# Optimization experiments

Measured on AMD Instinct MI355X. Metric: run time of the kernel, lower is better.

The kernel has to match this reference:

```python
import jax, jax.numpy as jnp
import numpy as np
from jax.ops import segment_sum

N_NODES = 50000
N_EDGES = 800000
IN_CH = 128
HID = 256
N_CLASSES = 10
N_GRAPHS = 64


def setup_inputs() -> dict:
    key = jax.random.key(0)
    ks = jax.random.split(key, 12)
    x = jax.random.normal(ks[0], (N_NODES, IN_CH), dtype=jnp.float32)
    edge_index = jax.random.randint(ks[1], (2, N_EDGES), 0, N_NODES, dtype=jnp.int64)
    batch = jnp.sort(jax.random.randint(ks[2], (N_NODES,), 0, N_GRAPHS, dtype=jnp.int64))
    def glorot(k, shape):
        lim = (6.0 / (shape[0] + shape[1])) ** 0.5
        return jax.random.uniform(k, shape, jnp.float32, -lim, lim)
    # GraphConv has two linear maps: lin_rel (neighbor aggregate, with bias) and lin_root (self)
    params = {
        "W1_root": glorot(ks[3], (IN_CH, HID)),  "W1_nbr": glorot(ks[4], (IN_CH, HID)),  "b1": jnp.zeros((HID,), jnp.float32),
        "W2_root": glorot(ks[5], (HID, HID)),    "W2_nbr": glorot(ks[6], (HID, HID)),    "b2": jnp.zeros((HID,), jnp.float32),
        "W3_root": glorot(ks[7], (HID, HID)),    "W3_nbr": glorot(ks[8], (HID, HID)),    "b3": jnp.zeros((HID,), jnp.float32),
        "W_lin": glorot(ks[9], (HID, N_CLASSES)), "b_lin": jnp.zeros((N_CLASSES,), jnp.float32),
    }
    return {"x": x, "edge_index": edge_index, "batch": batch, **params}


def _graph_conv(x, src, dst, W_root, W_nbr, b):
    # out_i = W_root x_i + W_nbr * sum_{j: (j->i) in E} x_j + b   (PyG GraphConv, aggr='add')
    agg = segment_sum(x[src], dst, num_segments=N_NODES)  # [N, d]
    return x @ W_root + agg @ W_nbr + b


def reference(x, edge_index, batch,
              W1_root, W1_nbr, b1,
              W2_root, W2_nbr, b2,
              W3_root, W3_nbr, b3,
              W_lin, b_lin):
    src, dst = edge_index[0], edge_index[1]
    h = jax.nn.relu(_graph_conv(x, src, dst, W1_root, W1_nbr, b1))
    h = jax.nn.relu(_graph_conv(h, src, dst, W2_root, W2_nbr, b2))
    h = _graph_conv(h, src, dst, W3_root, W3_nbr, b3)
    # global_mean_pool over graph ids
    sums = segment_sum(h, batch, num_segments=N_GRAPHS)                        # [G, HID]
    counts = segment_sum(jnp.ones((h.shape[0],), h.dtype), batch, num_segments=N_GRAPHS)
    pooled = sums / jnp.maximum(counts, 1.0)[:, None]
    # dropout is identity at inference
    return pooled @ W_lin + b_lin  # [G, n_classes]
```

## Files before the change

### kernel.cpp

```cpp
#include <hip/hip_runtime.h>
#include <stdint.h>

#define N_NODES 50000
#define N_EDGES 800000
#define IN_CH 128
#define HID 256
#define N_GRAPHS 64
#define N_CLASSES 10

#define GEMM_WG ((N_NODES + 127) / 128)
#define NB ((N_NODES + 127) / 128)
#define EPB 4096
#define CAP 4096

typedef unsigned short u16;
typedef __attribute__((ext_vector_type(8))) short short8;
typedef __attribute__((ext_vector_type(4))) float f32x4;

__device__ __forceinline__ float bf2f(uint32_t u) {
    union { uint32_t i; float f; } v; v.i = u << 16; return v.f;
}
__device__ __forceinline__ uint32_t f2bf(float f) {
    union { float f; uint32_t i; } v; v.f = f;
    return (v.i + 0x7FFFu + ((v.i >> 16) & 1u)) >> 16;
}

__global__ void __launch_bounds__(512) bin_pass(const int* __restrict__ src,
                                                const int* __restrict__ dst,
                                                int* __restrict__ gcnt,
                                                uint32_t* __restrict__ tmp)
{
    __shared__ int hist[NB];
    __shared__ int base[NB];
    int t = threadIdx.x;
    for (int i = t; i < NB; i += 512) hist[i] = 0;
    __syncthreads();
    const int e0 = blockIdx.x * EPB;
    int b_[8], s_[8], d_[8];
    #pragma unroll
    for (int k = 0; k < 8; ++k) {
        int e = e0 + k * 512 + t;
        if (e < N_EDGES) {
            int d = dst[e];
            b_[k] = d >> 7;
            d_[k] = d & 127;
            s_[k] = src[e];
            atomicAdd(&hist[b_[k]], 1);
        } else b_[k] = -1;
    }
    __syncthreads();
    for (int i = t; i < NB; i += 512) {
        int c = hist[i];
        base[i] = c ? atomicAdd(&gcnt[i], c) : 0;
        hist[i] = 0;
    }
    __syncthreads();
    #pragma unroll
    for (int k = 0; k < 8; ++k) {
        if (b_[k] >= 0) {
            int r = atomicAdd(&hist[b_[k]], 1);
            int pos = base[b_[k]] + r;
            if (pos < CAP)
                tmp[(size_t)b_[k] * CAP + pos] = ((uint32_t)s_[k] << 7) | (uint32_t)d_[k];
        }
    }
}

__global__ void __launch_bounds__(512) bucket_scan(const int* __restrict__ gcnt,
                                                   int* __restrict__ boff,
                                                   int* __restrict__ row_start)
{
    __shared__ int buf[512];
    int t = threadIdx.x;
    int v = (t < NB) ? gcnt[t] : 0;
    buf[t] = v;
    __syncthreads();
    #pragma unroll
    for (int off = 1; off < 512; off <<= 1) {
        int a = (t >= off) ? buf[t - off] : 0;
        __syncthreads();
        buf[t] += a;
        __syncthreads();
    }
    if (t < NB) boff[t] = buf[t] - v;
    if (t == 0) row_start[N_NODES] = N_EDGES;
}

__global__ void __launch_bounds__(256) debin2(const uint32_t* __restrict__ tmp,
                                              const int* __restrict__ gcnt,
                                              const int* __restrict__ boff,
                                              int* __restrict__ row_start,
                                              int* __restrict__ esrc)
{
    __shared__ int h[128];
    __shared__ int pre[128];
    __shared__ int cur[128];
    const int b = blockIdx.x;
    const int n0 = b * 128;
    const int nn = min(128, N_NODES - n0);
    const int t = threadIdx.x;
    const int cnt = min(gcnt[b], CAP);
    const int bb = boff[b];
    const uint32_t* te = tmp + (size_t)b * CAP;

    if (t < 128) h[t] = 0;
    __syncthreads();
    for (int p = t; p < cnt; p += 256)
        atomicAdd(&h[te[p] & 127u], 1);
    __syncthreads();
    if (t < 128) pre[t] = h[t];
    __syncthreads();
    #pragma unroll
    for (int off = 1; off < 128; off <<= 1) {
        int a = (t >= off && t < 128) ? pre[t - off] : 0;
        __syncthreads();
        if (t < 128) pre[t] += a;
        __syncthreads();
    }
    if (t < nn) {
        int rs = bb + pre[t] - h[t];
        row_start[n0 + t] = rs;
        cur[t] = rs;
    }
    __syncthreads();
    for (int p = t; p < cnt; p += 256) {
        uint32_t v = te[p];
        int pos = atomicAdd(&cur[v & 127u], 1);
        esrc[pos] = (int)(v >> 7);
    }
}

#define XB 3125
__global__ void __launch_bounds__(256)
cvt_all(const float* __restrict__ x, u16* __restrict__ xb,
        const float* __restrict__ W1r, const float* __restrict__ W1n,
        const float* __restrict__ W2r, const float* __restrict__ W2n,
        const float* __restrict__ W3r, const float* __restrict__ W3n,
        u16* __restrict__ o1r, u16* __restrict__ o1n,
        u16* __restrict__ o2r, u16* __restrict__ o2n,
        u16* __restrict__ o3r, u16* __restrict__ o3n)
{
    if (blockIdx.x < XB) {
        int id = blockIdx.x * 256 + threadIdx.x;
        const float4 a = *reinterpret_cast<const float4*>(x + (size_t)id * 8);
        const float4 b = *reinterpret_cast<const float4*>(x + (size_t)id * 8 + 4);
        uint4 o;
        o.x = f2bf(a.x) | (f2bf(a.y) << 16);
        o.y = f2bf(a.z) | (f2bf(a.w) << 16);
        o.z = f2bf(b.x) | (f2bf(b.y) << 16);
        o.w = f2bf(b.z) | (f2bf(b.w) << 16);
        *reinterpret_cast<uint4*>(xb + (size_t)id * 8) = o;
        return;
    }
    int id = (blockIdx.x - XB) * 256 + threadIdx.x;
    if (id < 65536) {
        int m = id >> 15;
        int r = id & 32767;
        int k = r >> 8, n = r & 255;
        const float* W = m ? W1n : W1r;
        u16* O = m ? o1n : o1r;
        O[n * 128 + k] = (u16)f2bf(W[r]);
    } else {
        id -= 65536;
        int m = id >> 16;
        int r = id & 65535;
        int k = r >> 8, n = r & 255;
        const float* W = (m == 0) ? W2r : (m == 1) ? W2n : (m == 2) ? W3r : W3n;
        u16* O = (m == 0) ? o2r : (m == 1) ? o2n : (m == 2) ? o3r : o3n;
        O[n * 256 + k] = (u16)f2bf(W[r]);
    }
}

template<int D, int NPH>
__global__ void __launch_bounds__(256)
gather_ph(const u16* __restrict__ feat, const int* __restrict__ row_start,
          const int* __restrict__ esrc, u16* __restrict__ agg)
{
    constexpr int CW = D / NPH;
    constexpr int GS = CW / 8;
    constexpr int NPB = 256 / GS;
    const int node = blockIdx.x * NPB + threadIdx.x / GS;
    const int lane = threadIdx.x % GS;
    const bool act = node < N_NODES;
    int s = 0, e = 0;
    if (act) { s = row_start[node]; e = row_start[node + 1]; }

    #pragma unroll
    for (int p = 0; p < NPH; ++p) {
        const u16* fp = feat + p * CW + lane * 8;
        float acc[8] = {0.f, 0.f, 0.f, 0.f, 0.f, 0.f, 0.f, 0.f};
        auto add = [&](uint4 v) {
            acc[0] += bf2f(v.x & 0xFFFF); acc[1] += bf2f(v.x >> 16);
            acc[2] += bf2f(v.y & 0xFFFF); acc[3] += bf2f(v.y >> 16);
            acc[4] += bf2f(v.z & 0xFFFF); acc[5] += bf2f(v.z >> 16);
            acc[6] += bf2f(v.w & 0xFFFF); acc[7] += bf2f(v.w >> 16);
        };
        int j = s;
        for (; j + 3 < e; j += 4) {
            int s0 = esrc[j], s1 = esrc[j + 1], s2 = esrc[j + 2], s3 = esrc[j + 3];
            uint4 v0 = *reinterpret_cast<const uint4*>(fp + (size_t)s0 * D);
            uint4 v1 = *reinterpret_cast<const uint4*>(fp + (size_t)s1 * D);
            uint4 v2 = *reinterpret_cast<const uint4*>(fp + (size_t)s2 * D);
            uint4 v3 = *reinterpret_cast<const uint4*>(fp + (size_t)s3 * D);
            add(v0); add(v1); add(v2); add(v3);
        }
        for (; j < e; ++j) {
            uint4 v0 = *reinterpret_cast<const uint4*>(fp + (size_t)esrc[j] * D);
            add(v0);
        }
        if (act) {
            uint4 o;
            o.x = f2bf(acc[0]) | (f2bf(acc[1]) << 16);
            o.y = f2bf(acc[2]) | (f2bf(acc[3]) << 16);
            o.z = f2bf(acc[4]) | (f2bf(acc[5]) << 16);
            o.w = f2bf(acc[6]) | (f2bf(acc[7]) << 16);
            *reinterpret_cast<uint4*>(agg + (size_t)node * D + p * CW + lane * 8) = o;
        }
        if (p + 1 < NPH) __syncthreads();
    }
}

template<int RELU>
__global__ void __launch_bounds__(512)
mfma_gemm(const u16* __restrict__ A1, const u16* __restrict__ A2,
          const u16* __restrict__ B1t, const u16* __restrict__ B2t,
          const float* __restrict__ bias,
          u16* __restrict__ C,
          int M, int K)
{
    __shared__ __align__(16) u16 As[128][40];
    __shared__ __align__(16) u16 Bs[256][40];

    const int orig = blockIdx.x;
    const int q = GEMM_WG / 8, r = GEMM_WG % 8;
    const int xcd = orig % 8;
    const int wg = (xcd < r ? xcd * (q + 1) : r * (q + 1) + (xcd - r) * q) + orig / 8;

    const int tid = threadIdx.x;
    const int bm = wg * 128;
    const int w  = tid >> 6;
    const int wm = (w >> 2) * 64;
    const int wn = (w & 3) * 64;
    const int l  = tid & 63;
    const int lr = l & 15;
    const int kb = (l >> 4) * 8;

    f32x4 acc[4][4];
    #pragma unroll
    for (int i = 0; i < 4; ++i)
        #pragma unroll
        for (int j = 0; j < 4; ++j)
            acc[i][j] = (f32x4){0.f, 0.f, 0.f, 0.f};

    const int row_s = tid >> 2;
    const int c8    = (tid & 3) * 8;

    for (int mat = 0; mat < 2; ++mat) {
        const u16* __restrict__ Ag = mat ? A2 : A1;
        const u16* __restrict__ Bg = mat ? B2t : B1t;
        for (int k0 = 0; k0 < K; k0 += 32) {
            {
                uint4 va = make_uint4(0u, 0u, 0u, 0u);
                int gr = bm + row_s;
                if (gr < M)
                    va = *reinterpret_cast<const uint4*>(Ag + (size_t)gr * K + k0 + c8);
                *reinterpret_cast<uint4*>(&As[row_s][c8]) = va;
            }
            #pragma unroll
            for (int it = 0; it < 2; ++it) {
                int row = row_s + it * 128;
                uint4 vb = *reinterpret_cast<const uint4*>(Bg + (size_t)row * K + k0 + c8);
                *reinterpret_cast<uint4*>(&Bs[row][c8]) = vb;
            }
            __syncthreads();
            short8 af[4], bfr[4];
            #pragma unroll
            for (int f = 0; f < 4; ++f) {
                af[f]  = *reinterpret_cast<const short8*>(&As[wm + f * 16 + lr][kb]);
                bfr[f] = *reinterpret_cast<const short8*>(&Bs[wn + f * 16 + lr][kb]);
            }
            #pragma unroll
            for (int fm = 0; fm < 4; ++fm)
                #pragma unroll
                for (int fn = 0; fn < 4; ++fn)
                    acc[fm][fn] = __builtin_amdgcn_mfma_f32_16x16x32_bf16(
                        af[fm], bfr[fn], acc[fm][fn], 0, 0, 0);
            __syncthreads();
        }
    }

    const int r4 = (l >> 4) * 4;
    #pragma unroll
    for (int fm = 0; fm < 4; ++fm) {
        #pragma unroll
        for (int rr = 0; rr < 4; ++rr) {
            int row = bm + wm + fm * 16 + r4 + rr;
            if (row >= M) continue;
            #pragma unroll
            for (int fn = 0; fn < 4; ++fn) {
                int col = wn + fn * 16 + lr;
                float v = acc[fm][fn][rr] + bias[col];
                if (RELU) v = fmaxf(v, 0.f);
                C[(size_t)row * HID + col] = (u16)f2bf(v);
            }
        }
    }
}

__device__ __forceinline__ int lower_bound_g(const int* __restrict__ batch, int g)
{
    int lo = 0, hi = N_NODES;
    while (lo < hi) {
        int mid = (lo + hi) >> 1;
        if (batch[mid] < g) lo = mid + 1; else hi = mid;
    }
    return lo;
}

__global__ void pool1_kernel(const u16* __restrict__ h, const int* __restrict__ batch,
                             float* __restrict__ partial)
{
    int g = blockIdx.x >> 3;
    int c = blockIdx.x & 7;
    int t = threadIdx.x;
    int s = lower_bound_g(batch, g);
    int e = lower_bound_g(batch, g + 1);
    int cnt = e - s;
    int a = s + (int)(((long long)cnt * c) >> 3);
    int b = s + (int)(((long long)cnt * (c + 1)) >> 3);
    float acc = 0.f;
    for (int i = a; i < b; ++i)
        acc += bf2f(h[(size_t)i * HID + t]);
    partial[(size_t)blockIdx.x * HID + t] = acc;
}

__global__ void pool2_final(const float* __restrict__ partial, const int* __restrict__ batch,
                            const float* __restrict__ W_lin, const float* __restrict__ b_lin,
                            float* __restrict__ out)
{
    __shared__ float v[HID];
    int g = blockIdx.x;
    int t = threadIdx.x;
    float acc = 0.f;
    #pragma unroll
    for (int c = 0; c < 8; ++c)
        acc += partial[(size_t)(g * 8 + c) * HID + t];
    float cnt = fmaxf((float)(lower_bound_g(batch, g + 1) - lower_bound_g(batch, g)), 1.f);
    v[t] = acc / cnt;
    __syncthreads();
    if (t < N_CLASSES) {
        float s = b_lin[t];
        for (int k = 0; k < HID; ++k)
            s += v[k] * W_lin[k * N_CLASSES + t];
        out[g * N_CLASSES + t] = s;
    }
}

extern "C" void kernel_launch(void* const* d_in, const int* in_sizes, int n_in,
                              void* d_out, int out_size, void* d_ws, size_t ws_size,
                              hipStream_t stream)
{
    const float* x     = (const float*)d_in[0];
    const int*   ei    = (const int*)d_in[1];
    const int*   batch = (const int*)d_in[2];
    const float* W1r = (const float*)d_in[3];
    const float* W1n = (const float*)d_in[4];
    const float* b1  = (const float*)d_in[5];
    const float* W2r = (const float*)d_in[6];
    const float* W2n = (const float*)d_in[7];
    const float* b2  = (const float*)d_in[8];
    const float* W3r = (const float*)d_in[9];
    const float* W3n = (const float*)d_in[10];
    const float* b3  = (const float*)d_in[11];
    const float* Wl  = (const float*)d_in[12];
    const float* bl  = (const float*)d_in[13];
    float* out = (float*)d_out;

    const int* src = ei;
    const int* dst = ei + N_EDGES;

    char* base = (char*)d_ws;
    size_t off = 0;
    auto alloc = [&](size_t bytes) { char* p = base + off; off += (bytes + 255) & ~(size_t)255; return p; };
    u16* x_bf = (u16*)alloc((size_t)N_NODES * IN_CH * 2);
    u16* hA   = (u16*)alloc((size_t)N_NODES * HID * 2);
    u16* hB   = (u16*)alloc((size_t)N_NODES * HID * 2);
    u16* agg  = (u16*)alloc((size_t)N_NODES * HID * 2);
    u16* wt1r = (u16*)alloc((size_t)HID * IN_CH * 2);
    u16* wt1n = (u16*)alloc((size_t)HID * IN_CH * 2);
    u16* wt2r = (u16*)alloc((size_t)HID * HID * 2);
    u16* wt2n = (u16*)alloc((size_t)HID * HID * 2);
    u16* wt3r = (u16*)alloc((size_t)HID * HID * 2);
    u16* wt3n = (u16*)alloc((size_t)HID * HID * 2);
    float* partial = (float*)alloc((size_t)N_GRAPHS * 8 * HID * 4);
    int* row_start = (int*)alloc((size_t)(N_NODES + 1) * 4);
    int* esrc      = (int*)alloc((size_t)N_EDGES * 4);
    uint32_t* tmp  = (uint32_t*)alloc((size_t)NB * CAP * 4);
    int* gcnt      = (int*)alloc((size_t)NB * 4);
    int* boff      = (int*)alloc((size_t)NB * 4);

    hipMemsetAsync(gcnt, 0, NB * sizeof(int), stream);
    bin_pass<<<(N_EDGES + EPB - 1) / EPB, 512, 0, stream>>>(src, dst, gcnt, tmp);
    bucket_scan<<<1, 512, 0, stream>>>(gcnt, boff, row_start);
    debin2<<<NB, 256, 0, stream>>>(tmp, gcnt, boff, row_start, esrc);

    cvt_all<<<XB + 1280, 256, 0, stream>>>(x, x_bf, W1r, W1n, W2r, W2n, W3r, W3n,
                                           wt1r, wt1n, wt2r, wt2n, wt3r, wt3n);

    const int G128 = (N_NODES + 31) / 32;
    const int G256 = (N_NODES + 15) / 16;

    gather_ph<IN_CH, 2><<<G128, 256, 0, stream>>>(x_bf, row_start, esrc, agg);
    mfma_gemm<1><<<GEMM_WG, 512, 0, stream>>>(x_bf, agg, wt1r, wt1n, b1, hA, N_NODES, IN_CH);

    gather_ph<HID, 2><<<G256, 256, 0, stream>>>(hA, row_start, esrc, agg);
    mfma_gemm<1><<<GEMM_WG, 512, 0, stream>>>(hA, agg, wt2r, wt2n, b2, hB, N_NODES, HID);

    gather_ph<HID, 2><<<G256, 256, 0, stream>>>(hB, row_start, esrc, agg);
    mfma_gemm<0><<<GEMM_WG, 512, 0, stream>>>(hB, agg, wt3r, wt3n, b3, hA, N_NODES, HID);

    pool1_kernel<<<N_GRAPHS * 8, HID, 0, stream>>>(hA, batch, partial);
    pool2_final<<<N_GRAPHS, HID, 0, stream>>>(partial, batch, Wl, bl, out);
}
```

Before: 302.7 us.

## Store node features in blocked pair-chunk layout and split gather by column chunk

Node feature matrices are now stored in a blocked layout where two consecutive nodes share a 128-byte block per 32-column chunk. The gather kernel assigns each block a single 32-column chunk across 64 nodes, so each gathered neighbour read is a 64-byte contiguous piece, and concurrent blocks touch a smaller working set per chunk. The GEMMs read the root operand in blocked layout and, for the first two layers, write their output in blocked form. The costs are scattered 2-byte stores in the GEMM epilogue and more gather blocks that each reread the row_start and esrc lists.

New measurement: 344.0 us. +13.6%, slower.

```diff
diff --git a/kernel.cpp b/kernel.cpp
--- a/kernel.cpp
+++ b/kernel.cpp
@@ -12,6 +12,7 @@
 #define NB ((N_NODES + 127) / 128)
 #define EPB 4096
 #define CAP 4096
+#define GTILES ((N_NODES + 63) / 64)
 
 typedef unsigned short u16;
 typedef __attribute__((ext_vector_type(8))) short short8;
@@ -23,6 +24,10 @@
 __device__ __forceinline__ uint32_t f2bf(float f) {
     union { float f; uint32_t i; } v; v.f = f;
     return (v.i + 0x7FFFu + ((v.i >> 16) & 1u)) >> 16;
+}
+
+__device__ __forceinline__ size_t blk_idx(int node, int col, int nch) {
+    return ((size_t)(node >> 1) * nch + (col >> 5)) * 64 + (node & 1) * 32 + (col & 31);
 }
 
 __global__ void __launch_bounds__(512) bin_pass(const int* __restrict__ src,
@@ -132,7 +137,7 @@
 
 #define XB 3125
 __global__ void __launch_bounds__(256)
-cvt_all(const float* __restrict__ x, u16* __restrict__ xb,
+cvt_all(const float* __restrict__ x, u16* __restrict__ xblk,
         const float* __restrict__ W1r, const float* __restrict__ W1n,
         const float* __restrict__ W2r, const float* __restrict__ W2n,
         const float* __restrict__ W3r, const float* __restrict__ W3n,
@@ -142,6 +147,8 @@
 {
     if (blockIdx.x < XB) {
         int id = blockIdx.x * 256 + threadIdx.x;
+        int node = id >> 4;
+        int col0 = (id & 15) * 8;
         const float4 a = *reinterpret_cast<const float4*>(x + (size_t)id * 8);
         const float4 b = *reinterpret_cast<const float4*>(x + (size_t)id * 8 + 4);
         uint4 o;
@@ -149,7 +156,7 @@
         o.y = f2bf(a.z) | (f2bf(a.w) << 16);
         o.z = f2bf(b.x) | (f2bf(b.y) << 16);
         o.w = f2bf(b.z) | (f2bf(b.w) << 16);
-        *reinterpret_cast<uint4*>(xb + (size_t)id * 8) = o;
+        *reinterpret_cast<uint4*>(xblk + blk_idx(node, col0, IN_CH / 32)) = o;
         return;
     }
     int id = (blockIdx.x - XB) * 256 + threadIdx.x;
@@ -171,62 +178,57 @@
     }
 }
 
-template<int D, int NPH>
+template<int D>
 __global__ void __launch_bounds__(256)
-gather_ph(const u16* __restrict__ feat, const int* __restrict__ row_start,
-          const int* __restrict__ esrc, u16* __restrict__ agg)
-{
-    constexpr int CW = D / NPH;
-    constexpr int GS = CW / 8;
-    constexpr int NPB = 256 / GS;
-    const int node = blockIdx.x * NPB + threadIdx.x / GS;
-    const int lane = threadIdx.x % GS;
-    const bool act = node < N_NODES;
-    int s = 0, e = 0;
-    if (act) { s = row_start[node]; e = row_start[node + 1]; }
-
-    #pragma unroll
-    for (int p = 0; p < NPH; ++p) {
-        const u16* fp = feat + p * CW + lane * 8;
-        float acc[8] = {0.f, 0.f, 0.f, 0.f, 0.f, 0.f, 0.f, 0.f};
-        auto add = [&](uint4 v) {
-            acc[0] += bf2f(v.x & 0xFFFF); acc[1] += bf2f(v.x >> 16);
-            acc[2] += bf2f(v.y & 0xFFFF); acc[3] += bf2f(v.y >> 16);
-            acc[4] += bf2f(v.z & 0xFFFF); acc[5] += bf2f(v.z >> 16);
-            acc[6] += bf2f(v.w & 0xFFFF); acc[7] += bf2f(v.w >> 16);
-        };
-        int j = s;
-        for (; j + 3 < e; j += 4) {
-            int s0 = esrc[j], s1 = esrc[j + 1], s2 = esrc[j + 2], s3 = esrc[j + 3];
-            uint4 v0 = *reinterpret_cast<const uint4*>(fp + (size_t)s0 * D);
-            uint4 v1 = *reinterpret_cast<const uint4*>(fp + (size_t)s1 * D);
-            uint4 v2 = *reinterpret_cast<const uint4*>(fp + (size_t)s2 * D);
-            uint4 v3 = *reinterpret_cast<const uint4*>(fp + (size_t)s3 * D);
-            add(v0); add(v1); add(v2); add(v3);
-        }
-        for (; j < e; ++j) {
-            uint4 v0 = *reinterpret_cast<const uint4*>(fp + (size_t)esrc[j] * D);
-            add(v0);
-        }
-        if (act) {
-            uint4 o;
-            o.x = f2bf(acc[0]) | (f2bf(acc[1]) << 16);
-            o.y = f2bf(acc[2]) | (f2bf(acc[3]) << 16);
-            o.z = f2bf(acc[4]) | (f2bf(acc[5]) << 16);
-            o.w = f2bf(acc[6]) | (f2bf(acc[7]) << 16);
-            *reinterpret_cast<uint4*>(agg + (size_t)node * D + p * CW + lane * 8) = o;
-        }
-        if (p + 1 < NPH) __syncthreads();
-    }
-}
-
-template<int RELU>
+gather_blk(const u16* __restrict__ feat, const int* __restrict__ row_start,
+           const int* __restrict__ esrc, u16* __restrict__ agg)
+{
+    constexpr int NCH = D / 32;
+    const int chunk = blockIdx.x & (NCH - 1);
+    const int tile  = blockIdx.x / NCH;
+    const int node  = tile * 64 + (threadIdx.x >> 2);
+    const int lane  = threadIdx.x & 3;
+    if (node >= N_NODES) return;
+    const int s = row_start[node], e = row_start[node + 1];
+    float acc[8] = {0.f, 0.f, 0.f, 0.f, 0.f, 0.f, 0.f, 0.f};
+    const u16* fp = feat + (size_t)chunk * 64 + lane * 8;
+
+    auto addr = [&](int sj) {
+        return reinterpret_cast<const uint4*>(fp + ((size_t)(sj >> 1) * NCH) * 64 + (sj & 1) * 32);
+    };
+    auto add = [&](uint4 v) {
+        acc[0] += bf2f(v.x & 0xFFFF); acc[1] += bf2f(v.x >> 16);
+        acc[2] += bf2f(v.y & 0xFFFF); acc[3] += bf2f(v.y >> 16);
+        acc[4] += bf2f(v.z & 0xFFFF); acc[5] += bf2f(v.z >> 16);
+        acc[6] += bf2f(v.w & 0xFFFF); acc[7] += bf2f(v.w >> 16);
+    };
+
+    int j = s;
+    for (; j + 3 < e; j += 4) {
+        uint4 v0 = *addr(esrc[j]);
+        uint4 v1 = *addr(esrc[j + 1]);
+        uint4 v2 = *addr(esrc[j + 2]);
+        uint4 v3 = *addr(esrc[j + 3]);
+        add(v0); add(v1); add(v2); add(v3);
+    }
+    for (; j < e; ++j)
+        add(*addr(esrc[j]));
+
+    uint4 o;
+    o.x = f2bf(acc[0]) | (f2bf(acc[1]) << 16);
+    o.y = f2bf(acc[2]) | (f2bf(acc[3]) << 16);
+    o.z = f2bf(acc[4]) | (f2bf(acc[5]) << 16);
+    o.w = f2bf(acc[6]) | (f2bf(acc[7]) << 16);
+    *reinterpret_cast<uint4*>(agg + (size_t)node * D + chunk * 32 + lane * 8) = o;
+}
+
+template<int RELU, int K, int BLKOUT>
 __global__ void __launch_bounds__(512)
 mfma_gemm(const u16* __restrict__ A1, const u16* __restrict__ A2,
           const u16* __restrict__ B1t, const u16* __restrict__ B2t,
           const float* __restrict__ bias,
           u16* __restrict__ C,
-          int M, int K)
+          int M)
 {
     __shared__ __align__(16) u16 As[128][40];
     __shared__ __align__(16) u16 Bs[256][40];
@@ -262,8 +264,13 @@
             {
                 uint4 va = make_uint4(0u, 0u, 0u, 0u);
                 int gr = bm + row_s;
-                if (gr < M)
-                    va = *reinterpret_cast<const uint4*>(Ag + (size_t)gr * K + k0 + c8);
+                int col = k0 + c8;
+                if (gr < M) {
+                    if (mat == 0)
+                        va = *reinterpret_cast<const uint4*>(Ag + blk_idx(gr, col, K / 32));
+                    else
+                        va = *reinterpret_cast<const uint4*>(Ag + (size_t)gr * K + col);
+                }
                 *reinterpret_cast<uint4*>(&As[row_s][c8]) = va;
             }
             #pragma unroll
@@ -301,7 +308,10 @@
                 int col = wn + fn * 16 + lr;
                 float v = acc[fm][fn][rr] + bias[col];
                 if (RELU) v = fmaxf(v, 0.f);
-                C[(size_t)row * HID + col] = (u16)f2bf(v);
+                if (BLKOUT)
+                    C[blk_idx(row, col, HID / 32)] = (u16)f2bf(v);
+                else
+                    C[(size_t)row * HID + col] = (u16)f2bf(v);
             }
         }
     }
@@ -382,10 +392,10 @@
     char* base = (char*)d_ws;
     size_t off = 0;
     auto alloc = [&](size_t bytes) { char* p = base + off; off += (bytes + 255) & ~(size_t)255; return p; };
-    u16* x_bf = (u16*)alloc((size_t)N_NODES * IN_CH * 2);
-    u16* hA   = (u16*)alloc((size_t)N_NODES * HID * 2);
-    u16* hB   = (u16*)alloc((size_t)N_NODES * HID * 2);
-    u16* agg  = (u16*)alloc((size_t)N_NODES * HID * 2);
+    u16* x_blk = (u16*)alloc((size_t)N_NODES * IN_CH * 2);
+    u16* h1b   = (u16*)alloc((size_t)N_NODES * HID * 2);
+    u16* h2b   = (u16*)alloc((size_t)N_NODES * HID * 2);
+    u16* agg   = (u16*)alloc((size_t)N_NODES * HID * 2);
     u16* wt1r = (u16*)alloc((size_t)HID * IN_CH * 2);
     u16* wt1n = (u16*)alloc((size_t)HID * IN_CH * 2);
     u16* wt2r = (u16*)alloc((size_t)HID * HID * 2);
@@ -399,26 +409,25 @@
     int* gcnt      = (int*)alloc((size_t)NB * 4);
     int* boff      = (int*)alloc((size_t)NB * 4);
 
+    u16* h3 = h1b;
+
     hipMemsetAsync(gcnt, 0, NB * sizeof(int), stream);
     bin_pass<<<(N_EDGES + EPB - 1) / EPB, 512, 0, stream>>>(src, dst, gcnt, tmp);
     bucket_scan<<<1, 512, 0, stream>>>(gcnt, boff, row_start);
     debin2<<<NB, 256, 0, stream>>>(tmp, gcnt, boff, row_start, esrc);
 
-    cvt_all<<<XB + 1280, 256, 0, stream>>>(x, x_bf, W1r, W1n, W2r, W2n, W3r, W3n,
+    cvt_all<<<XB + 1280, 256, 0, stream>>>(x, x_blk, W1r, W1n, W2r, W2n, W3r, W3n,
                                            wt1r, wt1n, wt2r, wt2n, wt3r, wt3n);
 
-    const int G128 = (N_NODES + 31) / 32;
-    const int G256 = (N_NODES + 15) / 16;
-
-    gather_ph<IN_CH, 2><<<G128, 256, 0, stream>>>(x_bf, row_start, esrc, agg);
-    mfma_gemm<1><<<GEMM_WG, 512, 0, stream>>>(x_bf, agg, wt1r, wt1n, b1, hA, N_NODES, IN_CH);
-
-    gather_ph<HID, 2><<<G256, 256, 0, stream>>>(hA, row_start, esrc, agg);
-    mfma_gemm<1><<<GEMM_WG, 512, 0, stream>>>(hA, agg, wt2r, wt2n, b2, hB, N_NODES, HID);
-
-    gather_ph<HID, 2><<<G256, 256, 0, stream>>>(hB, row_start, esrc, agg);
-    mfma_gemm<0><<<GEMM_WG, 512, 0, stream>>>(hB, agg, wt3r, wt3n, b3, hA, N_NODES, HID);
-
-    pool1_kernel<<<N_GRAPHS * 8, HID, 0, stream>>>(hA, batch, partial);
+    gather_blk<IN_CH><<<GTILES * (IN_CH / 32), 256, 0, stream>>>(x_blk, row_start, esrc, agg);
+    mfma_gemm<1, IN_CH, 1><<<GEMM_WG, 512, 0, stream>>>(x_blk, agg, wt1r, wt1n, b1, h1b, N_NODES);
+
+    gather_blk<HID><<<GTILES * (HID / 32), 256, 0, stream>>>(h1b, row_start, esrc, agg);
+    mfma_gemm<1, HID, 1><<<GEMM_WG, 512, 0, stream>>>(h1b, agg, wt2r, wt2n, b2, h2b, N_NODES);
+
+    gather_blk<HID><<<GTILES * (HID / 32), 256, 0, stream>>>(h2b, row_start, esrc, agg);
+    mfma_gemm<0, HID, 0><<<GEMM_WG, 512, 0, stream>>>(h2b, agg, wt3r, wt3n, b3, h3, N_NODES);
+
+    pool1_kernel<<<N_GRAPHS * 8, HID, 0, stream>>>(h3, batch, partial);
     pool2_final<<<N_GRAPHS, HID, 0, stream>>>(partial, batch, Wl, bl, out);
 }
```

## Fuse neighbor gather into GEMM, keeping aggregates in shared memory

Applied to the files above, without the earlier changes.

Replaces the separate gather and dual-GEMM kernels per layer with one kernel. Each 64-row workgroup first gathers neighbor sums into shared memory, then runs the root and neighbor GEMMs, reading the aggregate straight from LDS. This drops the global write and re-read of the aggregate buffer and halves the launches per layer. In exchange the tile shrinks from 128 to 64 rows, so weight tiles are reloaded more often, and LDS use rises, which may limit occupancy. The gather phase also cannot overlap with MFMA work inside a block.

Result: slower. 329.3 us, median of 2 (+8.8%).

```diff
diff --git a/kernel.cpp b/kernel.cpp
--- a/kernel.cpp
+++ b/kernel.cpp
@@ -8,7 +8,7 @@
 #define N_GRAPHS 64
 #define N_CLASSES 10
 
-#define GEMM_WG ((N_NODES + 127) / 128)
+#define FUSED_WG ((N_NODES + 63) / 64)
 #define NB ((N_NODES + 127) / 128)
 #define EPB 4096
 #define CAP 4096
@@ -171,127 +171,150 @@
     }
 }
 
-template<int D, int NPH>
-__global__ void __launch_bounds__(256)
-gather_ph(const u16* __restrict__ feat, const int* __restrict__ row_start,
-          const int* __restrict__ esrc, u16* __restrict__ agg)
-{
-    constexpr int CW = D / NPH;
-    constexpr int GS = CW / 8;
-    constexpr int NPB = 256 / GS;
-    const int node = blockIdx.x * NPB + threadIdx.x / GS;
-    const int lane = threadIdx.x % GS;
-    const bool act = node < N_NODES;
-    int s = 0, e = 0;
-    if (act) { s = row_start[node]; e = row_start[node + 1]; }
-
-    #pragma unroll
-    for (int p = 0; p < NPH; ++p) {
-        const u16* fp = feat + p * CW + lane * 8;
-        float acc[8] = {0.f, 0.f, 0.f, 0.f, 0.f, 0.f, 0.f, 0.f};
-        auto add = [&](uint4 v) {
-            acc[0] += bf2f(v.x & 0xFFFF); acc[1] += bf2f(v.x >> 16);
-            acc[2] += bf2f(v.y & 0xFFFF); acc[3] += bf2f(v.y >> 16);
-            acc[4] += bf2f(v.z & 0xFFFF); acc[5] += bf2f(v.z >> 16);
-            acc[6] += bf2f(v.w & 0xFFFF); acc[7] += bf2f(v.w >> 16);
-        };
-        int j = s;
-        for (; j + 3 < e; j += 4) {
-            int s0 = esrc[j], s1 = esrc[j + 1], s2 = esrc[j + 2], s3 = esrc[j + 3];
-            uint4 v0 = *reinterpret_cast<const uint4*>(fp + (size_t)s0 * D);
-            uint4 v1 = *reinterpret_cast<const uint4*>(fp + (size_t)s1 * D);
-            uint4 v2 = *reinterpret_cast<const uint4*>(fp + (size_t)s2 * D);
-            uint4 v3 = *reinterpret_cast<const uint4*>(fp + (size_t)s3 * D);
-            add(v0); add(v1); add(v2); add(v3);
-        }
-        for (; j < e; ++j) {
-            uint4 v0 = *reinterpret_cast<const uint4*>(fp + (size_t)esrc[j] * D);
-            add(v0);
-        }
-        if (act) {
-            uint4 o;
-            o.x = f2bf(acc[0]) | (f2bf(acc[1]) << 16);
-            o.y = f2bf(acc[2]) | (f2bf(acc[3]) << 16);
-            o.z = f2bf(acc[4]) | (f2bf(acc[5]) << 16);
-            o.w = f2bf(acc[6]) | (f2bf(acc[7]) << 16);
-            *reinterpret_cast<uint4*>(agg + (size_t)node * D + p * CW + lane * 8) = o;
-        }
-        if (p + 1 < NPH) __syncthreads();
-    }
-}
-
-template<int RELU>
-__global__ void __launch_bounds__(512)
-mfma_gemm(const u16* __restrict__ A1, const u16* __restrict__ A2,
-          const u16* __restrict__ B1t, const u16* __restrict__ B2t,
-          const float* __restrict__ bias,
-          u16* __restrict__ C,
-          int M, int K)
-{
-    __shared__ __align__(16) u16 As[128][40];
+template<int RELU, int K>
+__global__ void __launch_bounds__(512, 4)
+fused_layer(const u16* __restrict__ feat,
+            const int* __restrict__ row_start,
+            const int* __restrict__ esrc,
+            const u16* __restrict__ B1t,
+            const u16* __restrict__ B2t,
+            const float* __restrict__ bias,
+            u16* __restrict__ C,
+            int M)
+{
+    __shared__ __align__(16) u16 agg[64][K + 8];
+    __shared__ __align__(16) u16 As[64][40];
     __shared__ __align__(16) u16 Bs[256][40];
 
     const int orig = blockIdx.x;
-    const int q = GEMM_WG / 8, r = GEMM_WG % 8;
+    const int q = FUSED_WG / 8, r = FUSED_WG % 8;
     const int xcd = orig % 8;
     const int wg = (xcd < r ? xcd * (q + 1) : r * (q + 1) + (xcd - r) * q) + orig / 8;
 
     const int tid = threadIdx.x;
-    const int bm = wg * 128;
+    const int bm = wg * 64;
+
+    {
+        constexpr int NCH = K / 2;
+        constexpr int LPN = NCH / 8;
+        constexpr int NPP = 512 / LPN;
+        constexpr int PASSES = 64 / NPP;
+        const int lane = tid % LPN;
+        const int nl0  = tid / LPN;
+
+        for (int h = 0; h < 2; ++h) {
+            const u16* fp = feat + h * NCH + lane * 8;
+            #pragma unroll
+            for (int p = 0; p < PASSES; ++p) {
+                const int nl = p * NPP + nl0;
+                const int node = bm + nl;
+                float acc[8] = {0.f, 0.f, 0.f, 0.f, 0.f, 0.f, 0.f, 0.f};
+                if (node < M) {
+                    const int s = row_start[node], e = row_start[node + 1];
+                    auto add = [&](uint4 v) {
+                        acc[0] += bf2f(v.x & 0xFFFF); acc[1] += bf2f(v.x >> 16);
+                        acc[2] += bf2f(v.y & 0xFFFF); acc[3] += bf2f(v.y >> 16);
+                        acc[4] += bf2f(v.z & 0xFFFF); acc[5] += bf2f(v.z >> 16);
+                        acc[6] += bf2f(v.w & 0xFFFF); acc[7] += bf2f(v.w >> 16);
+                    };
+                    int j = s;
+                    for (; j + 3 < e; j += 4) {
+                        int s0 = esrc[j], s1 = esrc[j + 1], s2 = esrc[j + 2], s3 = esrc[j + 3];
+                        uint4 v0 = *reinterpret_cast<const uint4*>(fp + (size_t)s0 * K);
+                        uint4 v1 = *reinterpret_cast<const uint4*>(fp + (size_t)s1 * K);
+                        uint4 v2 = *reinterpret_cast<const uint4*>(fp + (size_t)s2 * K);
+                        uint4 v3 = *reinterpret_cast<const uint4*>(fp + (size_t)s3 * K);
+                        add(v0); add(v1); add(v2); add(v3);
+                    }
+                    for (; j < e; ++j)
+                        add(*reinterpret_cast<const uint4*>(fp + (size_t)esrc[j] * K));
+                }
+                uint4 o;
+                o.x = f2bf(acc[0]) | (f2bf(acc[1]) << 16);
+                o.y = f2bf(acc[2]) | (f2bf(acc[3]) << 16);
+                o.z = f2bf(acc[4]) | (f2bf(acc[5]) << 16);
+                o.w = f2bf(acc[6]) | (f2bf(acc[7]) << 16);
+                *reinterpret_cast<uint4*>(&agg[nl][h * NCH + lane * 8]) = o;
+            }
+        }
+    }
+    __syncthreads();
+
     const int w  = tid >> 6;
-    const int wm = (w >> 2) * 64;
+    const int wm = (w >> 2) * 32;
     const int wn = (w & 3) * 64;
     const int l  = tid & 63;
     const int lr = l & 15;
     const int kb = (l >> 4) * 8;
 
-    f32x4 acc[4][4];
-    #pragma unroll
-    for (int i = 0; i < 4; ++i)
+    f32x4 acc[2][4];
+    #pragma unroll
+    for (int i = 0; i < 2; ++i)
         #pragma unroll
         for (int j = 0; j < 4; ++j)
             acc[i][j] = (f32x4){0.f, 0.f, 0.f, 0.f};
 
-    const int row_s = tid >> 2;
+    const int row_a = tid >> 2;
     const int c8    = (tid & 3) * 8;
 
-    for (int mat = 0; mat < 2; ++mat) {
-        const u16* __restrict__ Ag = mat ? A2 : A1;
-        const u16* __restrict__ Bg = mat ? B2t : B1t;
-        for (int k0 = 0; k0 < K; k0 += 32) {
-            {
-                uint4 va = make_uint4(0u, 0u, 0u, 0u);
-                int gr = bm + row_s;
-                if (gr < M)
-                    va = *reinterpret_cast<const uint4*>(Ag + (size_t)gr * K + k0 + c8);
-                *reinterpret_cast<uint4*>(&As[row_s][c8]) = va;
-            }
+    for (int k0 = 0; k0 < K; k0 += 32) {
+        if (tid < 256) {
+            uint4 va = make_uint4(0u, 0u, 0u, 0u);
+            int gr = bm + row_a;
+            if (gr < M)
+                va = *reinterpret_cast<const uint4*>(feat + (size_t)gr * K + k0 + c8);
+            *reinterpret_cast<uint4*>(&As[row_a][c8]) = va;
+        }
+        #pragma unroll
+        for (int it = 0; it < 2; ++it) {
+            int row = (tid >> 2) + it * 128;
+            uint4 vb = *reinterpret_cast<const uint4*>(B1t + (size_t)row * K + k0 + c8);
+            *reinterpret_cast<uint4*>(&Bs[row][c8]) = vb;
+        }
+        __syncthreads();
+        short8 af[2], bfr[4];
+        #pragma unroll
+        for (int f = 0; f < 2; ++f)
+            af[f] = *reinterpret_cast<const short8*>(&As[wm + f * 16 + lr][kb]);
+        #pragma unroll
+        for (int f = 0; f < 4; ++f)
+            bfr[f] = *reinterpret_cast<const short8*>(&Bs[wn + f * 16 + lr][kb]);
+        #pragma unroll
+        for (int fm = 0; fm < 2; ++fm)
             #pragma unroll
-            for (int it = 0; it < 2; ++it) {
-                int row = row_s + it * 128;
-                uint4 vb = *reinterpret_cast<const uint4*>(Bg + (size_t)row * K + k0 + c8);
-                *reinterpret_cast<uint4*>(&Bs[row][c8]) = vb;
-            }
-            __syncthreads();
-            short8 af[4], bfr[4];
+            for (int fn = 0; fn < 4; ++fn)
+                acc[fm][fn] = __builtin_amdgcn_mfma_f32_16x16x32_bf16(
+                    af[fm], bfr[fn], acc[fm][fn], 0, 0, 0);
+        __syncthreads();
+    }
+
+    for (int k0 = 0; k0 < K; k0 += 32) {
+        #pragma unroll
+        for (int it = 0; it < 2; ++it) {
+            int row = (tid >> 2) + it * 128;
+            uint4 vb = *reinterpret_cast<const uint4*>(B2t + (size_t)row * K + k0 + c8);
+            *reinterpret_cast<uint4*>(&Bs[row][c8]) = vb;
+        }
+        __syncthreads();
+        short8 af[2], bfr[4];
+        #pragma unroll
+        for (int f = 0; f < 2; ++f)
+            af[f] = *reinterpret_cast<const short8*>(&agg[wm + f * 16 + lr][k0 + kb]);
+        #pragma unroll
+        for (int f = 0; f < 4; ++f)
+            bfr[f] = *reinterpret_cast<const short8*>(&Bs[wn + f * 16 + lr][kb]);
+        #pragma unroll
+        for (int fm = 0; fm < 2; ++fm)
             #pragma unroll
-            for (int f = 0; f < 4; ++f) {
-                af[f]  = *reinterpret_cast<const short8*>(&As[wm + f * 16 + lr][kb]);
-                bfr[f] = *reinterpret_cast<const short8*>(&Bs[wn + f * 16 + lr][kb]);
-            }
-            #pragma unroll
-            for (int fm = 0; fm < 4; ++fm)
-                #pragma unroll
-                for (int fn = 0; fn < 4; ++fn)
-                    acc[fm][fn] = __builtin_amdgcn_mfma_f32_16x16x32_bf16(
-                        af[fm], bfr[fn], acc[fm][fn], 0, 0, 0);
-            __syncthreads();
-        }
+            for (int fn = 0; fn < 4; ++fn)
+                acc[fm][fn] = __builtin_amdgcn_mfma_f32_16x16x32_bf16(
+                    af[fm], bfr[fn], acc[fm][fn], 0, 0, 0);
+        __syncthreads();
     }
 
     const int r4 = (l >> 4) * 4;
     #pragma unroll
-    for (int fm = 0; fm < 4; ++fm) {
+    for (int fm = 0; fm < 2; ++fm) {
         #pragma unroll
         for (int rr = 0; rr < 4; ++rr) {
             int row = bm + wm + fm * 16 + r4 + rr;
@@ -385,7 +408,6 @@
     u16* x_bf = (u16*)alloc((size_t)N_NODES * IN_CH * 2);
     u16* hA   = (u16*)alloc((size_t)N_NODES * HID * 2);
     u16* hB   = (u16*)alloc((size_t)N_NODES * HID * 2);
-    u16* agg  = (u16*)alloc((size_t)N_NODES * HID * 2);
     u16* wt1r = (u16*)alloc((size_t)HID * IN_CH * 2);
     u16* wt1n = (u16*)alloc((size_t)HID * IN_CH * 2);
     u16* wt2r = (u16*)alloc((size_t)HID * HID * 2);
@@ -407,17 +429,12 @@
     cvt_all<<<XB + 1280, 256, 0, stream>>>(x, x_bf, W1r, W1n, W2r, W2n, W3r, W3n,
                                            wt1r, wt1n, wt2r, wt2n, wt3r, wt3n);
 
-    const int G128 = (N_NODES + 31) / 32;
-    const int G256 = (N_NODES + 15) / 16;
-
-    gather_ph<IN_CH, 2><<<G128, 256, 0, stream>>>(x_bf, row_start, esrc, agg);
-    mfma_gemm<1><<<GEMM_WG, 512, 0, stream>>>(x_bf, agg, wt1r, wt1n, b1, hA, N_NODES, IN_CH);
-
-    gather_ph<HID, 2><<<G256, 256, 0, stream>>>(hA, row_start, esrc, agg);
-    mfma_gemm<1><<<GEMM_WG, 512, 0, stream>>>(hA, agg, wt2r, wt2n, b2, hB, N_NODES, HID);
-
-    gather_ph<HID, 2><<<G256, 256, 0, stream>>>(hB, row_start, esrc, agg);
-    mfma_gemm<0><<<GEMM_WG, 512, 0, stream>>>(hB, agg, wt3r, wt3n, b3, hA, N_NODES, HID);
+    fused_layer<1, IN_CH><<<FUSED_WG, 512, 0, stream>>>(x_bf, row_start, esrc,
+                                                        wt1r, wt1n, b1, hA, N_NODES);
+    fused_layer<1, HID><<<FUSED_WG, 512, 0, stream>>>(hA, row_start, esrc,
+                                                      wt2r, wt2n, b2, hB, N_NODES);
+    fused_layer<0, HID><<<FUSED_WG, 512, 0, stream>>>(hB, row_start, esrc,
+                                                      wt3r, wt3n, b3, hA, N_NODES);
 
     pool1_kernel<<<N_GRAPHS * 8, HID, 0, stream>>>(hA, batch, partial);
     pool2_final<<<N_GRAPHS, HID, 0, stream>>>(partial, batch, Wl, bl, out);
```
